# Kernel tuning notes

Measured on AMD Instinct MI355X. Metric: run time of the kernel, lower is better.

The kernel has to match this reference:

```python
import jax, jax.numpy as jnp
import numpy as np


def setup_inputs() -> dict:
    key = jax.random.key(0)
    ks = jax.random.split(key, 6)
    B, T, E = 4, 1024, 1024
    H, D = 16, 64  # num_heads = embed_size // head_size
    s = 0.02
    x = jax.random.normal(ks[0], (B, T, E), dtype=jnp.float32)
    Wq = jax.random.normal(ks[1], (H, D, E), dtype=jnp.float32) * s
    Wk = jax.random.normal(ks[2], (H, D, E), dtype=jnp.float32) * s
    Wv = jax.random.normal(ks[3], (H, D, E), dtype=jnp.float32) * s
    Wp = jax.random.normal(ks[4], (E, E), dtype=jnp.float32) * s
    bp = jnp.zeros((E,), dtype=jnp.float32)
    return {"x": x, "Wq": Wq, "Wk": Wk, "Wv": Wv, "Wp": Wp, "bp": bp}


def reference(x, Wq, Wk, Wv, Wp, bp):
    # x: [B, T, E]; Wq/Wk/Wv: [H, D, E] (per-head Linear(E, D, bias=False) weights)
    B, T, E = x.shape
    H, D, _ = Wq.shape
    scale = 1.0 / jnp.sqrt(jnp.asarray(D, dtype=x.dtype))
    # per-head projections, vectorized over heads (same math as the ModuleList loop)
    q = jnp.einsum('bte,hde->bhtd', x, Wq)
    k = jnp.einsum('bte,hde->bhtd', x, Wk)
    v = jnp.einsum('bte,hde->bhtd', x, Wv)
    scores = jnp.einsum('bhtd,bhsd->bhts', q, k) * scale  # [B,H,T,T]
    causal = jnp.tril(jnp.ones((T, T), dtype=bool))
    scores = jnp.where(causal[None, None], scores, jnp.finfo(x.dtype).min)
    att = jax.nn.softmax(scores, axis=-1)  # attention dropout: identity in eval
    o = jnp.einsum('bhts,bhsd->bhtd', att, v)
    # concat heads along channel dim (head order = module list order)
    o = o.transpose(0, 2, 1, 3).reshape(B, T, H * D)
    # output projection (nn.Linear: y = o @ Wp.T + bp); dropout: identity in eval
    return o @ Wp.T + bp
```

## Files before the change

### kernel.cpp

```cpp
#include <hip/hip_runtime.h>


#define T_SZ 1024
#define E_SZ 1024
#define H_SZ 16
#define D_SZ 64

typedef __attribute__((ext_vector_type(8))) short bf16x8;
typedef __attribute__((ext_vector_type(4))) short bf16x4;
typedef __attribute__((ext_vector_type(4))) float f32x4;

static __device__ __forceinline__ unsigned short f2b(float f) {
  unsigned int u = __builtin_bit_cast(unsigned int, f);
  u += 0x7fffu + ((u >> 16) & 1u);
  return (unsigned short)(u >> 16);
}

static __device__ __forceinline__ unsigned int cvt_pk(float lo, float hi) {
  unsigned int r;
  asm("v_cvt_pk_bf16_f32 %0, %1, %2" : "=v"(r) : "v"(lo), "v"(hi));
  return r;
}

static __device__ __forceinline__ void load_lds16(const void* g, void* l) {
  __builtin_amdgcn_global_load_lds(
      (const __attribute__((address_space(1))) void*)g,
      (__attribute__((address_space(3))) void*)l, 16, 0, 0);
}

__global__ void cast_all(const float* __restrict__ x, const float* __restrict__ wq,
                         const float* __restrict__ wk, const float* __restrict__ wv,
                         const float* __restrict__ wp,
                         unsigned short* __restrict__ xb,
                         unsigned short* __restrict__ wqkvb,
                         unsigned short* __restrict__ wpb) {
  int b = blockIdx.x;
  const float4* src;
  ushort4* dst;
  int i;
  if (b < 4096) {
    src = (const float4*)x; dst = (ushort4*)xb; i = b * 256 + threadIdx.x;
  } else {
    int a = (b - 4096) >> 10;
    i = ((b - 4096) & 1023) * 256 + threadIdx.x;
    src = (const float4*)(a == 0 ? wq : a == 1 ? wk : a == 2 ? wv : wp);
    dst = (ushort4*)(a == 3 ? wpb : wqkvb + (size_t)a * 1048576);
  }
  float4 v = src[i];
  ushort4 o;
  o.x = f2b(v.x); o.y = f2b(v.y); o.z = f2b(v.z); o.w = f2b(v.w);
  dst[i] = o;
}

template <int EPI>
__global__ void gemm_bt(const unsigned short* __restrict__ A,
                        const unsigned short* __restrict__ Bm,
                        int M, int N, int K,
                        float* __restrict__ outF, const float* __restrict__ bias,
                        unsigned short* __restrict__ Qb,
                        unsigned short* __restrict__ Kb,
                        unsigned short* __restrict__ Vb) {
  __shared__ __align__(16) char lds[32768];
  const int tid = threadIdx.x;
  const int wid = tid >> 6;
  const int lane = tid & 63;
  const int llo = lane & 15, lhi = lane >> 4;
  const int row0 = blockIdx.x * 128, col0 = blockIdx.y * 128;
  const int wr = (wid >> 1) * 64, wc = (wid & 1) * 64;

  f32x4 acc[4][4];
#pragma unroll
  for (int m = 0; m < 4; ++m)
#pragma unroll
    for (int n = 0; n < 4; ++n) {
      f32x4 z = {0.f, 0.f, 0.f, 0.f};
      acc[m][n] = z;
    }

  auto stage = [&](int kt, char* base) {
#pragma unroll
    for (int c = 0; c < 2; ++c) {
      int off = c * 4096 + tid * 16;
      int r = off >> 6, cb = off & 63;
      load_lds16((const char*)A + ((size_t)(row0 + r) * K + kt) * 2 + cb,
                 base + c * 4096 + wid * 1024);
      load_lds16((const char*)Bm + ((size_t)(col0 + r) * K + kt) * 2 + cb,
                 base + 8192 + c * 4096 + wid * 1024);
    }
  };

  stage(0, lds);
  __syncthreads();
  int buf = 0;

  for (int kt = 0; kt < K; kt += 32) {
    char* cur = lds + buf * 16384;
    if (kt + 32 < K) stage(kt + 32, lds + (buf ^ 1) * 16384);

    bf16x8 af[4], bfr[4];
#pragma unroll
    for (int m = 0; m < 4; ++m)
      af[m] = *reinterpret_cast<const bf16x8*>(cur + (wr + m * 16 + llo) * 64 + lhi * 16);
#pragma unroll
    for (int n = 0; n < 4; ++n)
      bfr[n] = *reinterpret_cast<const bf16x8*>(cur + 8192 + (wc + n * 16 + llo) * 64 + lhi * 16);
#pragma unroll
    for (int m = 0; m < 4; ++m)
#pragma unroll
      for (int n = 0; n < 4; ++n)
        acc[m][n] = __builtin_amdgcn_mfma_f32_16x16x32_bf16(af[m], bfr[n], acc[m][n], 0, 0, 0);
    __syncthreads();
    buf ^= 1;
  }

#pragma unroll
  for (int m = 0; m < 4; ++m)
#pragma unroll
    for (int n = 0; n < 4; ++n)
#pragma unroll
      for (int r = 0; r < 4; ++r) {
        int grow = row0 + wr + m * 16 + lhi * 4 + r;
        int gcol = col0 + wc + n * 16 + llo;
        float v = acc[m][n][r];
        if (EPI == 0) {
          int b = grow >> 10, t = grow & 1023;
          int which = gcol >> 10, hd = gcol & 1023;
          int h = hd >> 6, d = hd & 63;
          unsigned short* dst = (which == 0) ? Qb : (which == 1) ? Kb : Vb;
          dst[(((size_t)(b * H_SZ + h)) * T_SZ + t) * D_SZ + d] = f2b(v);
        } else {
          outF[(size_t)grow * N + gcol] = v + bias[gcol];
        }
      }
}

__global__ void transpose_v(const unsigned short* __restrict__ Vb,
                            unsigned short* __restrict__ Vtb) {
  __shared__ unsigned short tile[64 * 71 + 8];
  const int tid = threadIdx.x;
  const int bh = blockIdx.y;
  const int t0 = blockIdx.x * 64;
  const size_t base = (size_t)bh * (T_SZ * D_SZ);
#pragma unroll
  for (int u = 0; u < 2; ++u) {
    int cid = u * 256 + tid;
    int r = cid >> 3, ck = cid & 7;
    bf16x8 v = *reinterpret_cast<const bf16x8*>(Vb + base + (size_t)(t0 + r) * D_SZ + ck * 8);
#pragma unroll
    for (int j = 0; j < 8; ++j)
      tile[(ck * 8 + j) * 71 + r] = (unsigned short)v[j];
  }
  __syncthreads();
#pragma unroll
  for (int u = 0; u < 2; ++u) {
    int cid = u * 256 + tid;
    int d = cid >> 3, tc = cid & 7;
    bf16x8 o;
#pragma unroll
    for (int j = 0; j < 8; ++j)
      o[j] = (short)tile[d * 71 + tc * 8 + j];
    *reinterpret_cast<bf16x8*>(Vtb + base + (size_t)d * T_SZ + t0 + tc * 8) = o;
  }
}

__global__ void attn_kernel(const unsigned short* __restrict__ Q,
                            const unsigned short* __restrict__ K,
                            const unsigned short* __restrict__ Vt,
                            unsigned short* __restrict__ O) {
  __shared__ __align__(16) char smem[32768];
  const int tid = threadIdx.x, wid = tid >> 6, lane = tid & 63;
  const int llo = lane & 15, lhi = lane >> 4;
  const int fid = blockIdx.y * 8 + blockIdx.x;
  const int wi = (fid & 7) * 64 + (fid >> 3);
  const int blkx = wi & 7;
  const int bh = wi >> 3;
  const size_t bhbase = (size_t)bh * (T_SZ * D_SZ);
  char* Ks = smem;
  char* Vs = smem + 8192;
  char* Ps = smem + 16384 + wid * 2048;

  const int qrow = blkx * 128 + wid * 16 + llo;
  const int myqt = 2 * blkx + (wid >> 2);
  const int last = 2 * blkx + 1;
  bf16x8 bq[2];
  {
    const unsigned short* qp = Q + bhbase + (size_t)qrow * D_SZ + lhi * 8;
    bq[0] = *reinterpret_cast<const bf16x8*>(qp);
    bq[1] = *reinterpret_cast<const bf16x8*>(qp + 32);
  }

  const int soff = tid * 16;
  const int srow = soff >> 7;
  const int sinb = soff & 127;
  const int slds = srow * 128 + (sinb ^ ((srow & 7) << 4));

  bf16x8 kreg, vreg;
  kreg = *reinterpret_cast<const bf16x8*>(K + bhbase + (size_t)srow * D_SZ + (sinb >> 1));
  vreg = *reinterpret_cast<const bf16x8*>(Vt + bhbase + (size_t)srow * T_SZ + (sinb >> 1));

  f32x4 oacc[4];
#pragma unroll
  for (int dc = 0; dc < 4; ++dc) {
    f32x4 z = {0.f, 0.f, 0.f, 0.f};
    oacc[dc] = z;
  }
  float mrun = -1e30f, lrun = 0.f;
  const float scale = 0.125f;

  for (int it = 0; it <= last; ++it) {
    __syncthreads();
    *reinterpret_cast<bf16x8*>(Ks + slds) = kreg;
    *reinterpret_cast<bf16x8*>(Vs + slds) = vreg;
    if (it < last) {
      const int kv = (it + 1) * 64;
      kreg = *reinterpret_cast<const bf16x8*>(
          K + bhbase + (size_t)(kv + srow) * D_SZ + (sinb >> 1));
      vreg = *reinterpret_cast<const bf16x8*>(
          Vt + bhbase + (size_t)srow * T_SZ + kv + (sinb >> 1));
    }
    __syncthreads();

    const int kv = it * 64;
    if (it <= myqt) {
      f32x4 sacc[4];
#pragma unroll
      for (int c = 0; c < 4; ++c) { f32x4 z = {0.f, 0.f, 0.f, 0.f}; sacc[c] = z; }
      __builtin_amdgcn_s_setprio(1);
#pragma unroll
      for (int seg = 0; seg < 2; ++seg)
#pragma unroll
        for (int c = 0; c < 4; ++c) {
          int key = c * 16 + llo;
          bf16x8 ak = *reinterpret_cast<const bf16x8*>(
              Ks + key * 128 + ((seg * 64 + lhi * 16) ^ ((key & 7) << 4)));
          sacc[c] = __builtin_amdgcn_mfma_f32_16x16x32_bf16(ak, bq[seg], sacc[c], 0, 0, 0);
        }
      __builtin_amdgcn_s_setprio(0);

      const bool diag = (it == myqt);
      float p[4][4];
      float pm = -1e30f;
#pragma unroll
      for (int c = 0; c < 4; ++c)
#pragma unroll
        for (int r = 0; r < 4; ++r) {
          float s = sacc[c][r] * scale;
          if (diag && (kv + c * 16 + lhi * 4 + r > qrow)) s = -1e30f;
          p[c][r] = s;
          pm = fmaxf(pm, s);
        }
      pm = fmaxf(pm, __shfl_xor(pm, 16, 64));
      pm = fmaxf(pm, __shfl_xor(pm, 32, 64));
      if (!__all(pm - mrun <= 8.0f)) {
        float mnew = fmaxf(mrun, pm);
        float alpha = __expf(mrun - mnew);
        mrun = mnew;
        lrun *= alpha;
#pragma unroll
        for (int dc = 0; dc < 4; ++dc)
#pragma unroll
          for (int r = 0; r < 4; ++r) oacc[dc][r] *= alpha;
      }

      float ps = 0.f;
#pragma unroll
      for (int c = 0; c < 4; ++c) {
#pragma unroll
        for (int r = 0; r < 4; ++r) {
          p[c][r] = __expf(p[c][r] - mrun);
          ps += p[c][r];
        }
        unsigned int w0 = cvt_pk(p[c][0], p[c][1]);
        unsigned int w1 = cvt_pk(p[c][2], p[c][3]);
        unsigned long long packed = ((unsigned long long)w1 << 32) | w0;
        *reinterpret_cast<bf16x4*>(
            Ps + llo * 128 + ((c * 32 + lhi * 8) ^ ((llo & 7) << 4))) =
            __builtin_bit_cast(bf16x4, packed);
      }
      asm volatile("s_waitcnt lgkmcnt(0)" ::: "memory");
      __builtin_amdgcn_sched_barrier(0);

      ps += __shfl_xor(ps, 16, 64);
      ps += __shfl_xor(ps, 32, 64);
      lrun += ps;

      __builtin_amdgcn_s_setprio(1);
#pragma unroll
      for (int seg = 0; seg < 2; ++seg) {
        bf16x8 bp = *reinterpret_cast<const bf16x8*>(
            Ps + llo * 128 + ((seg * 64 + lhi * 16) ^ ((llo & 7) << 4)));
#pragma unroll
        for (int dc = 0; dc < 4; ++dc) {
          int d = dc * 16 + llo;
          bf16x8 av = *reinterpret_cast<const bf16x8*>(
              Vs + d * 128 + ((seg * 64 + lhi * 16) ^ ((d & 7) << 4)));
          oacc[dc] = __builtin_amdgcn_mfma_f32_16x16x32_bf16(av, bp, oacc[dc], 0, 0, 0);
        }
      }
      __builtin_amdgcn_s_setprio(0);
    }
  }

  const int b = bh >> 4, h = bh & 15;
  float inv = 1.f / lrun;
#pragma unroll
  for (int dc = 0; dc < 4; ++dc) {
    unsigned int w0 = cvt_pk(oacc[dc][0] * inv, oacc[dc][1] * inv);
    unsigned int w1 = cvt_pk(oacc[dc][2] * inv, oacc[dc][3] * inv);
    unsigned int* op = reinterpret_cast<unsigned int*>(
        O + ((size_t)b * T_SZ + qrow) * E_SZ + h * D_SZ + dc * 16 + lhi * 4);
    op[0] = w0;
    op[1] = w1;
  }
}

extern "C" void kernel_launch(void* const* d_in, const int* in_sizes, int n_in,
                              void* d_out, int out_size, void* d_ws, size_t ws_size,
                              hipStream_t stream) {
  const float* x  = (const float*)d_in[0];
  const float* Wq = (const float*)d_in[1];
  const float* Wk = (const float*)d_in[2];
  const float* Wv = (const float*)d_in[3];
  const float* Wp = (const float*)d_in[4];
  const float* bp = (const float*)d_in[5];
  float* out = (float*)d_out;

  char* ws = (char*)d_ws;
  unsigned short* xb   = (unsigned short*)(ws);
  unsigned short* wqkv = (unsigned short*)(ws + (8u << 20));
  unsigned short* wp   = (unsigned short*)(ws + (14u << 20));
  unsigned short* Qb   = (unsigned short*)(ws + (16u << 20));
  unsigned short* Kb   = (unsigned short*)(ws + (24u << 20));
  unsigned short* Vb   = (unsigned short*)(ws + (32u << 20));
  unsigned short* Ob   = (unsigned short*)(ws + (40u << 20));
  unsigned short* Vtb  = xb;

  cast_all<<<8192, 256, 0, stream>>>(x, Wq, Wk, Wv, Wp, xb, wqkv, wp);

  gemm_bt<0><<<dim3(32, 24), 256, 0, stream>>>(xb, wqkv, 4096, 3072, 1024,
                                               nullptr, nullptr, Qb, Kb, Vb);
  transpose_v<<<dim3(16, 64), 256, 0, stream>>>(Vb, Vtb);
  attn_kernel<<<dim3(8, 64), 512, 0, stream>>>(Qb, Kb, Vtb, Ob);
  gemm_bt<1><<<dim3(32, 8), 256, 0, stream>>>(Ob, wp, 4096, 1024, 1024,
                                              out, bp, nullptr, nullptr, nullptr);
}
```

Baseline: 100.4 us.

## Triple-buffer GEMM LDS pipeline with swizzled layout and finer waitcnt barriers

The bf16 GEMM kernel moves from double to triple buffering in LDS, keeping two K-tiles of global-to-LDS loads in flight. The full __syncthreads is replaced by explicit vmcnt waits plus s_barrier, and K becomes a compile-time template parameter. It also XOR-swizzles the 16-byte column chunks by row, both when loading into LDS and when reading fragments, to reduce LDS bank conflicts. The cost is 48KB of LDS per block, which may lower occupancy, plus hand-written waitcnt counts that must match the number of outstanding loads.

Result: no change. 99.57 us (-0.8%).

```diff
diff --git a/kernel.cpp b/kernel.cpp
--- a/kernel.cpp
+++ b/kernel.cpp
@@ -52,15 +52,16 @@
   dst[i] = o;
 }
 
-template <int EPI>
+template <int EPI, int KT>
 __global__ void gemm_bt(const unsigned short* __restrict__ A,
                         const unsigned short* __restrict__ Bm,
-                        int M, int N, int K,
+                        int M, int N,
                         float* __restrict__ outF, const float* __restrict__ bias,
                         unsigned short* __restrict__ Qb,
                         unsigned short* __restrict__ Kb,
                         unsigned short* __restrict__ Vb) {
-  __shared__ __align__(16) char lds[32768];
+  constexpr int NT = KT / 32;
+  __shared__ __align__(16) char lds[49152];
   const int tid = threadIdx.x;
   const int wid = tid >> 6;
   const int lane = tid & 63;
@@ -77,40 +78,57 @@
       acc[m][n] = z;
     }
 
-  auto stage = [&](int kt, char* base) {
+  auto stage = [&](int j, char* base) {
 #pragma unroll
     for (int c = 0; c < 2; ++c) {
       int off = c * 4096 + tid * 16;
       int r = off >> 6, cb = off & 63;
-      load_lds16((const char*)A + ((size_t)(row0 + r) * K + kt) * 2 + cb,
+      int sb = cb ^ (((r >> 1) & 3) << 4);
+      load_lds16((const char*)A + ((size_t)(row0 + r) * KT + j * 32) * 2 + sb,
                  base + c * 4096 + wid * 1024);
-      load_lds16((const char*)Bm + ((size_t)(col0 + r) * K + kt) * 2 + cb,
+      load_lds16((const char*)Bm + ((size_t)(col0 + r) * KT + j * 32) * 2 + sb,
                  base + 8192 + c * 4096 + wid * 1024);
     }
   };
 
   stage(0, lds);
-  __syncthreads();
-  int buf = 0;
-
-  for (int kt = 0; kt < K; kt += 32) {
-    char* cur = lds + buf * 16384;
-    if (kt + 32 < K) stage(kt + 32, lds + (buf ^ 1) * 16384);
+  stage(1, lds + 16384);
+  asm volatile("s_waitcnt vmcnt(4)" ::: "memory");
+  __builtin_amdgcn_s_barrier();
+  asm volatile("" ::: "memory");
+  __builtin_amdgcn_sched_barrier(0);
+
+#pragma unroll 1
+  for (int i = 0; i < NT; ++i) {
+    char* cur = lds + (i % 3) * 16384;
+    if (i + 2 < NT) stage(i + 2, lds + ((i + 2) % 3) * 16384);
 
     bf16x8 af[4], bfr[4];
 #pragma unroll
-    for (int m = 0; m < 4; ++m)
-      af[m] = *reinterpret_cast<const bf16x8*>(cur + (wr + m * 16 + llo) * 64 + lhi * 16);
-#pragma unroll
-    for (int n = 0; n < 4; ++n)
-      bfr[n] = *reinterpret_cast<const bf16x8*>(cur + 8192 + (wc + n * 16 + llo) * 64 + lhi * 16);
+    for (int m = 0; m < 4; ++m) {
+      int row = wr + m * 16 + llo;
+      af[m] = *reinterpret_cast<const bf16x8*>(
+          cur + row * 64 + ((lhi * 16) ^ (((row >> 1) & 3) << 4)));
+    }
+#pragma unroll
+    for (int n = 0; n < 4; ++n) {
+      int row = wc + n * 16 + llo;
+      bfr[n] = *reinterpret_cast<const bf16x8*>(
+          cur + 8192 + row * 64 + ((lhi * 16) ^ (((row >> 1) & 3) << 4)));
+    }
 #pragma unroll
     for (int m = 0; m < 4; ++m)
 #pragma unroll
       for (int n = 0; n < 4; ++n)
         acc[m][n] = __builtin_amdgcn_mfma_f32_16x16x32_bf16(af[m], bfr[n], acc[m][n], 0, 0, 0);
-    __syncthreads();
-    buf ^= 1;
+
+    if (i + 1 < NT) {
+      if (i + 2 < NT) asm volatile("s_waitcnt vmcnt(4)" ::: "memory");
+      else            asm volatile("s_waitcnt vmcnt(0)" ::: "memory");
+      __builtin_amdgcn_s_barrier();
+      asm volatile("" ::: "memory");
+      __builtin_amdgcn_sched_barrier(0);
+    }
   }
 
 #pragma unroll
@@ -337,10 +355,10 @@
 
   cast_all<<<8192, 256, 0, stream>>>(x, Wq, Wk, Wv, Wp, xb, wqkv, wp);
 
-  gemm_bt<0><<<dim3(32, 24), 256, 0, stream>>>(xb, wqkv, 4096, 3072, 1024,
-                                               nullptr, nullptr, Qb, Kb, Vb);
+  gemm_bt<0, 1024><<<dim3(32, 24), 256, 0, stream>>>(xb, wqkv, 4096, 3072,
+                                                     nullptr, nullptr, Qb, Kb, Vb);
   transpose_v<<<dim3(16, 64), 256, 0, stream>>>(Vb, Vtb);
   attn_kernel<<<dim3(8, 64), 512, 0, stream>>>(Qb, Kb, Vtb, Ob);
-  gemm_bt<1><<<dim3(32, 8), 256, 0, stream>>>(Ob, wp, 4096, 1024, 1024,
-                                              out, bp, nullptr, nullptr, nullptr);
-}
+  gemm_bt<1, 1024><<<dim3(32, 8), 256, 0, stream>>>(Ob, wp, 4096, 1024,
+                                                    out, bp, nullptr, nullptr, nullptr);
+}
```
